# Kernel tuning notes

Hardware: AMD Instinct MI355X
Metric: run time of the kernel (lower is better)

The kernel has to match this reference:

```python
import jax, jax.numpy as jnp
import numpy as np

N_NODE = 20000
N_EDGE = 200000
EMBED = 256
PAIR = 128
HEADS = 16
HEAD_DIM = EMBED // HEADS
SCALING = HEAD_DIM ** -0.5
EPS = 1e-5


def _ln(x, w, b):
    m = x.mean(-1, keepdims=True)
    v = ((x - m) ** 2).mean(-1, keepdims=True)
    return (x - m) / jnp.sqrt(v + EPS) * w + b


def setup_inputs() -> dict:
    key = jax.random.key(0)
    ks = jax.random.split(key, 12)
    inp = {
        "query": jax.random.normal(ks[0], (N_NODE, EMBED), jnp.float32),
        "edge_index": jax.random.randint(ks[1], (N_EDGE, 2), 0, N_NODE, jnp.int64 if jax.config.jax_enable_x64 else jnp.int32),
        "edge_diff": jax.random.normal(ks[2], (N_EDGE, 3), jnp.float32),
        "pair": jax.random.normal(ks[3], (N_EDGE, PAIR), jnp.float32),
        "ln_w": jnp.ones((EMBED,), jnp.float32),
        "ln_b": jnp.zeros((EMBED,), jnp.float32),
        "pln_w": jnp.ones((PAIR,), jnp.float32),
        "pln_b": jnp.zeros((PAIR,), jnp.float32),
        "Wq": jax.random.normal(ks[4], (EMBED, EMBED), jnp.float32) * 0.02,
        "Wk": jax.random.normal(ks[5], (EMBED, EMBED), jnp.float32) * 0.02,
        "Wv": jax.random.normal(ks[6], (EMBED, EMBED), jnp.float32) * 0.02,
        "Wb": jax.random.normal(ks[7], (HEADS, PAIR), jnp.float32) * 0.02,
        "bb": jnp.zeros((HEADS,), jnp.float32),
        "Wf1": jax.random.normal(ks[8], (1, EMBED), jnp.float32) * 0.02,
        "bf1": jnp.zeros((1,), jnp.float32),
        "Wf2": jax.random.normal(ks[9], (1, EMBED), jnp.float32) * 0.02,
        "bf2": jnp.zeros((1,), jnp.float32),
        "Wf3": jax.random.normal(ks[10], (1, EMBED), jnp.float32) * 0.02,
        "bf3": jnp.zeros((1,), jnp.float32),
    }
    return inp


def reference(query, edge_index, edge_diff, pair, ln_w, ln_b, pln_w, pln_b,
              Wq, Wk, Wv, Wb, bb, Wf1, bf1, Wf2, bf2, Wf3, bf3):
    n_node = query.shape[0]
    src = edge_index[:, 0]
    dst = edge_index[:, 1]

    qn = _ln(query, ln_w, ln_b)          # preln on node features
    pn = _ln(pair, pln_w, pln_b)         # preln on pair features

    q = (qn @ Wq.T).reshape(n_node, HEADS, HEAD_DIM)
    k = (qn @ Wk.T).reshape(n_node, HEADS, HEAD_DIM)
    v = (qn @ Wv.T).reshape(n_node, HEADS, HEAD_DIM)

    qe = q[src] * SCALING                # [E,H,D]
    ke = k[dst]
    ve = v[dst]

    logits = (qe * ke).sum(-1) + pn @ Wb.T + bb   # [E,H]

    # segment softmax over destination node (edge_index[:,0])
    seg_max = jax.ops.segment_max(logits, src, num_segments=n_node)  # [N,H]
    ex = jnp.exp(logits - seg_max[src])
    denom = jax.ops.segment_sum(ex, src, num_segments=n_node)
    probs = ex / denom[src]              # [E,H]

    # 3D-weighted scatter-sum: out[n,h,c,d] = sum_e probs[e,h]*diff[e,c]*v[e,h,d]
    w = probs[:, :, None] * edge_diff[:, None, :]                    # [E,H,3]
    contrib = w[:, :, :, None] * ve[:, :, None, :]                   # [E,H,3,D]
    x = jax.ops.segment_sum(contrib, src, num_segments=n_node)       # [N,H,3,D]
    x = x.transpose(0, 2, 1, 3).reshape(n_node, 3, EMBED)            # [N,3,H*D]

    f1 = x[:, 0, :] @ Wf1.T + bf1
    f2 = x[:, 1, :] @ Wf2.T + bf2
    f3 = x[:, 2, :] @ Wf3.T + bf3
    return jnp.concatenate([f1, f2, f3], axis=-1).astype(jnp.float32)
```

## Files before the change

kernel.cpp:

```cpp
#include <hip/hip_runtime.h>
#include <math.h>

#define N_NODE 20000
#define N_EDGE 200000
#define EMBED 256
#define PAIR 128
#define HEADS 16
#define HEAD_DIM 16
#define SCALING 0.25f
#define LNEPS 1e-5f

typedef unsigned short u16;
typedef unsigned int u32;
typedef __attribute__((ext_vector_type(8))) short bf16x8;
typedef __attribute__((ext_vector_type(4))) float f32x4;

#define WS_QKV   0
#define WS_QN    30720000
#define WS_WBF   40960000
#define WS_WW    41353216
#define WS_C0    41357312
#define WS_C1    41357376
#define WS_BIAS  41357440
#define WS_VW    54157440
#define WS_CNT   57997440
#define WS_CUR   58077440
#define WS_OFF   58157440
#define WS_DE    58237504

__device__ __forceinline__ u16 f2bf(float f) {
  u32 u = __float_as_uint(f);
  u32 r = (u + 0x7FFFu + ((u >> 16) & 1u)) >> 16;
  return (u16)r;
}
__device__ __forceinline__ float bl(u32 u) { return __uint_as_float(u << 16); }
__device__ __forceinline__ float bh(u32 u) { return __uint_as_float(u & 0xFFFF0000u); }

__device__ __forceinline__ float dot8(uint4 a, uint4 b) {
  float s = bl(a.x) * bl(b.x) + bh(a.x) * bh(b.x);
  s += bl(a.y) * bl(b.y) + bh(a.y) * bh(b.y);
  s += bl(a.z) * bl(b.z) + bh(a.z) * bh(b.z);
  s += bl(a.w) * bl(b.w) + bh(a.w) * bh(b.w);
  return s;
}

__global__ __launch_bounds__(256) void k1_pre_kernel(
    const float* __restrict__ query, const float* __restrict__ ln_w,
    const float* __restrict__ ln_b, u16* __restrict__ qn,
    int* __restrict__ counts, int* __restrict__ cur,
    const float* __restrict__ Wq, const float* __restrict__ Wk,
    const float* __restrict__ Wv, u16* __restrict__ Wbf,
    const float* __restrict__ pln_w, const float* __restrict__ pln_b,
    const float* __restrict__ Wb, const float* __restrict__ bb,
    u16* __restrict__ WWbf, float* __restrict__ c0, float* __restrict__ c1) {
  int bid = blockIdx.x;
  if (bid < 5000) {
    int z = bid * 256 + threadIdx.x;
    if (z < N_NODE) { counts[z] = 0; cur[z] = 0; }
    int node = bid * 4 + (threadIdx.x >> 6);
    int lane = threadIdx.x & 63;
    float4 a = *(const float4*)(query + (size_t)node * EMBED + lane * 4);
    float s = a.x + a.y + a.z + a.w;
    float s2 = a.x * a.x + a.y * a.y + a.z * a.z + a.w * a.w;
    #pragma unroll
    for (int off = 32; off > 0; off >>= 1) {
      s += __shfl_xor(s, off);
      s2 += __shfl_xor(s2, off);
    }
    float m = s * (1.0f / EMBED);
    float r = rsqrtf(s2 * (1.0f / EMBED) - m * m + LNEPS);
    float4 w4 = *(const float4*)(ln_w + lane * 4);
    float4 b4 = *(const float4*)(ln_b + lane * 4);
    ushort4 st;
    st.x = f2bf((a.x - m) * r * w4.x + b4.x);
    st.y = f2bf((a.y - m) * r * w4.y + b4.y);
    st.z = f2bf((a.z - m) * r * w4.z + b4.z);
    st.w = f2bf((a.w - m) * r * w4.w + b4.w);
    *(ushort4*)(qn + (size_t)node * EMBED + lane * 4) = st;
  } else if (bid < 5192) {
    int g4 = (bid - 5000) * 256 + threadIdx.x;
    int idx = g4 * 4;
    const float* src = (idx < 65536) ? Wq : (idx < 131072 ? Wk : Wv);
    float4 v = *(const float4*)(src + (idx & 65535));
    ushort4 st = {f2bf(v.x), f2bf(v.y), f2bf(v.z), f2bf(v.w)};
    *(ushort4*)(Wbf + idx) = st;
  } else if (threadIdx.x < 64) {
    int l = threadIdx.x;
    for (int h = 0; h < HEADS; h++) {
      int i0 = l * 2;
      float wb0 = Wb[h * PAIR + i0], wb1 = Wb[h * PAIR + i0 + 1];
      float ww0 = pln_w[i0] * wb0, ww1 = pln_w[i0 + 1] * wb1;
      WWbf[h * PAIR + i0] = f2bf(ww0);
      WWbf[h * PAIR + i0 + 1] = f2bf(ww1);
      float s1 = ww0 + ww1;
      float s0 = pln_b[i0] * wb0 + pln_b[i0 + 1] * wb1;
      #pragma unroll
      for (int off = 32; off > 0; off >>= 1) {
        s1 += __shfl_xor(s1, off);
        s0 += __shfl_xor(s0, off);
      }
      if (l == 0) {
        c1[h] = s1;
        c0[h] = s0 + bb[h];
      }
    }
  }
}

#define GP 264
__global__ __launch_bounds__(256, 2) void k2_gemm_hist_kernel(
    const u16* __restrict__ qn, const u16* __restrict__ Wbf,
    u16* __restrict__ qkv, const int* __restrict__ edge_index,
    int* __restrict__ counts) {
  __shared__ u16 As[64 * GP];
  __shared__ u16 Bs[64 * GP];
  int bid = blockIdx.x;
  if (bid >= 3756) {
    int e = (bid - 3756) * 256 + threadIdx.x;
    if (e < N_EDGE) atomicAdd(&counts[edge_index[e * 2]], 1);
    return;
  }
  int bx = bid % 313, by = bid / 313;
  int t = threadIdx.x;
  int wv = t >> 6, lane = t & 63;
  int quad = lane >> 4, l16 = lane & 15;
  int row0 = bx * 64, col0 = by * 64;
  #pragma unroll
  for (int j = 0; j < 8; j++) {
    int row = j * 8 + (t >> 5);
    int slot = t & 31;
    int ra = min(row0 + row, N_NODE - 1);
    uint4 va = *(const uint4*)(qn + (size_t)ra * 256 + slot * 8);
    *(uint4*)(&As[row * GP + slot * 8]) = va;
    uint4 vb = *(const uint4*)(Wbf + (size_t)(col0 + row) * 256 + slot * 8);
    *(uint4*)(&Bs[row * GP + slot * 8]) = vb;
  }
  __syncthreads();
  int mt = (wv >> 1) * 32, nt = (wv & 1) * 32;
  f32x4 acc[2][2];
  #pragma unroll
  for (int im = 0; im < 2; im++)
    #pragma unroll
    for (int in_ = 0; in_ < 2; in_++) acc[im][in_] = (f32x4){0.f, 0.f, 0.f, 0.f};
  #pragma unroll
  for (int sk = 0; sk < 8; sk++) {
    int ko = sk * 32 + quad * 8;
    bf16x8 a0 = *(const bf16x8*)(&As[(mt + l16) * GP + ko]);
    bf16x8 a1 = *(const bf16x8*)(&As[(mt + 16 + l16) * GP + ko]);
    bf16x8 b0 = *(const bf16x8*)(&Bs[(nt + l16) * GP + ko]);
    bf16x8 b1 = *(const bf16x8*)(&Bs[(nt + 16 + l16) * GP + ko]);
    acc[0][0] = __builtin_amdgcn_mfma_f32_16x16x32_bf16(a0, b0, acc[0][0], 0, 0, 0);
    acc[0][1] = __builtin_amdgcn_mfma_f32_16x16x32_bf16(a0, b1, acc[0][1], 0, 0, 0);
    acc[1][0] = __builtin_amdgcn_mfma_f32_16x16x32_bf16(a1, b0, acc[1][0], 0, 0, 0);
    acc[1][1] = __builtin_amdgcn_mfma_f32_16x16x32_bf16(a1, b1, acc[1][1], 0, 0, 0);
  }
  float scale = (col0 < 256) ? SCALING : 1.0f;
  #pragma unroll
  for (int im = 0; im < 2; im++) {
    #pragma unroll
    for (int in_ = 0; in_ < 2; in_++) {
      #pragma unroll
      for (int r = 0; r < 4; r++) {
        int grow = row0 + mt + im * 16 + quad * 4 + r;
        int gcol = col0 + nt + in_ * 16 + l16;
        if (grow < N_NODE)
          qkv[(size_t)grow * 768 + gcol] = f2bf(acc[im][in_][r] * scale);
      }
    }
  }
}

__global__ __launch_bounds__(1024) void scan_kernel(
    const int* __restrict__ counts, int* __restrict__ off) {
  __shared__ int part[1024];
  int t = threadIdx.x;
  int loc[20];
  int s = 0;
  #pragma unroll
  for (int i = 0; i < 20; i++) {
    int idx = t * 20 + i;
    int v = (idx < N_NODE) ? counts[idx] : 0;
    loc[i] = s;
    s += v;
  }
  part[t] = s;
  __syncthreads();
  int x = s;
  for (int o = 1; o < 1024; o <<= 1) {
    int y = (t >= o) ? part[t - o] : 0;
    __syncthreads();
    x += y;
    part[t] = x;
    __syncthreads();
  }
  int excl = x - s;
  #pragma unroll
  for (int i = 0; i < 20; i++) {
    int idx = t * 20 + i;
    if (idx < N_NODE) off[idx] = excl + loc[i];
  }
  if (t == 0) off[N_NODE] = N_EDGE;
}

#define PP 136
__global__ __launch_bounds__(256) void k4_bias_vw_scatter_kernel(
    const float* __restrict__ pair, const u16* __restrict__ WWbf,
    const float* __restrict__ c0g, const float* __restrict__ c1g,
    float* __restrict__ bias, const u16* __restrict__ qkv,
    const float* __restrict__ Wf1, const float* __restrict__ Wf2,
    const float* __restrict__ Wf3, float* __restrict__ vw,
    const int* __restrict__ edge_index, const int* __restrict__ off,
    int* __restrict__ cur, int2* __restrict__ de) {
  __shared__ u16 Ps[64 * PP];
  __shared__ u16 WWs[16 * PP];
  __shared__ float ms[64], rs[64], c0s[16], c1s[16];
  int bid = blockIdx.x;
  int t = threadIdx.x;
  if (bid >= 4375) {
    int e = (bid - 4375) * 256 + t;
    if (e < N_EDGE) {
      int src = edge_index[e * 2 + 0];
      int dst = edge_index[e * 2 + 1];
      int pos = off[src] + atomicAdd(&cur[src], 1);
      de[pos] = make_int2(dst, e);
    }
    return;
  }
  if (bid >= 3125) {
    int gid = (bid - 3125) * 256 + t;
    int n = gid >> 4, h = gid & 15;
    const uint4* vp = (const uint4*)(qkv + (size_t)n * 768 + 512 + h * 16);
    uint4 va = vp[0], vb = vp[1];
    float v[16];
    v[0] = bl(va.x); v[1] = bh(va.x); v[2] = bl(va.y); v[3] = bh(va.y);
    v[4] = bl(va.z); v[5] = bh(va.z); v[6] = bl(va.w); v[7] = bh(va.w);
    v[8] = bl(vb.x); v[9] = bh(vb.x); v[10] = bl(vb.y); v[11] = bh(vb.y);
    v[12] = bl(vb.z); v[13] = bh(vb.z); v[14] = bl(vb.w); v[15] = bh(vb.w);
    const float* wf[3] = {Wf1 + h * 16, Wf2 + h * 16, Wf3 + h * 16};
    #pragma unroll
    for (int c = 0; c < 3; c++) {
      float s = 0.f;
      #pragma unroll
      for (int d = 0; d < 16; d++) s += v[d] * wf[c][d];
      vw[(size_t)n * 48 + h * 3 + c] = s;
    }
    return;
  }
  int wv = t >> 6, lane = t & 63;
  int quad = lane >> 4, l16 = lane & 15;
  int e0 = bid * 64;
  #pragma unroll
  for (int j = 0; j < 8; j++) {
    int L = j * 256 + t;
    int row = L >> 5, slot = L & 31;
    float4 p = *(const float4*)(pair + (size_t)(e0 + row) * PAIR + slot * 4);
    ushort4 st = {f2bf(p.x), f2bf(p.y), f2bf(p.z), f2bf(p.w)};
    *(ushort4*)(&Ps[row * PP + slot * 4]) = st;
  }
  #pragma unroll
  for (int j = 0; j < 2; j++) {
    int L = j * 256 + t;
    int row = L >> 5, slot = L & 31;
    ushort4 w = *(const ushort4*)(WWbf + row * PAIR + slot * 4);
    *(ushort4*)(&WWs[row * PP + slot * 4]) = w;
  }
  if (t < 16) {
    c0s[t] = c0g[t];
    c1s[t] = c1g[t];
  }
  __syncthreads();
  {
    int row = t >> 2, qq = t & 3;
    float s = 0.f, s2 = 0.f;
    #pragma unroll
    for (int jj = 0; jj < 8; jj++) {
      ushort4 u = *(const ushort4*)(&Ps[row * PP + (qq * 8 + jj) * 4]);
      float x0 = __uint_as_float((u32)u.x << 16);
      float x1 = __uint_as_float((u32)u.y << 16);
      float x2 = __uint_as_float((u32)u.z << 16);
      float x3 = __uint_as_float((u32)u.w << 16);
      s += x0 + x1 + x2 + x3;
      s2 += x0 * x0 + x1 * x1 + x2 * x2 + x3 * x3;
    }
    s += __shfl_xor(s, 1); s += __shfl_xor(s, 2);
    s2 += __shfl_xor(s2, 1); s2 += __shfl_xor(s2, 2);
    if (qq == 0) {
      float m = s * (1.0f / PAIR);
      ms[row] = m;
      rs[row] = rsqrtf(s2 * (1.0f / PAIR) - m * m + LNEPS);
    }
  }
  __syncthreads();
  f32x4 acc = (f32x4){0.f, 0.f, 0.f, 0.f};
  #pragma unroll
  for (int sk = 0; sk < 4; sk++) {
    int ko = sk * 32 + quad * 8;
    bf16x8 a = *(const bf16x8*)(&Ps[(wv * 16 + l16) * PP + ko]);
    bf16x8 b = *(const bf16x8*)(&WWs[l16 * PP + ko]);
    acc = __builtin_amdgcn_mfma_f32_16x16x32_bf16(a, b, acc, 0, 0, 0);
  }
  #pragma unroll
  for (int r = 0; r < 4; r++) {
    int el = wv * 16 + quad * 4 + r;
    float bv = rs[el] * (acc[r] - ms[el] * c1s[l16]) + c0s[l16];
    bias[(size_t)(e0 + el) * HEADS + l16] = bv;
  }
}

__global__ __launch_bounds__(256) void seg_attn_kernel(
    const u16* __restrict__ qkv, const float* __restrict__ bias,
    const int* __restrict__ off, const int2* __restrict__ de,
    const float* __restrict__ vw, const float* __restrict__ edge_diff,
    const float* __restrict__ bf1, const float* __restrict__ bf2,
    const float* __restrict__ bf3, float* __restrict__ out) {
  int wv = threadIdx.x >> 6, lane = threadIdx.x & 63;
  int src = blockIdx.x * 4 + wv;
  int h = lane & 15, eslot = lane >> 4;
  int lo = off[src];
  int deg = off[src + 1] - lo;
  const uint4* qp = (const uint4*)(qkv + (size_t)src * 768 + h * 16);
  uint4 q0 = qp[0], q1 = qp[1];
  float exsum = 0.f, a0 = 0.f, a1 = 0.f, a2 = 0.f;
  for (int ei = eslot; ei < deg; ei += 4) {
    int2 d_e = de[lo + ei];
    const uint4* kp = (const uint4*)(qkv + (size_t)d_e.x * 768 + 256 + h * 16);
    float d = dot8(q0, kp[0]) + dot8(q1, kp[1]);
    float ex = __expf(d + bias[(size_t)d_e.y * HEADS + h]);
    exsum += ex;
    const float* vp = vw + (size_t)d_e.x * 48 + h * 3;
    const float* dp = edge_diff + (size_t)d_e.y * 3;
    a0 += ex * vp[0] * dp[0];
    a1 += ex * vp[1] * dp[1];
    a2 += ex * vp[2] * dp[2];
  }
  exsum += __shfl_xor(exsum, 16);
  exsum += __shfl_xor(exsum, 32);
  float rden = (exsum > 0.f) ? 1.0f / exsum : 0.f;
  a0 *= rden; a1 *= rden; a2 *= rden;
  #pragma unroll
  for (int o = 1; o < 64; o <<= 1) {
    a0 += __shfl_xor(a0, o);
    a1 += __shfl_xor(a1, o);
    a2 += __shfl_xor(a2, o);
  }
  if (lane == 0) {
    out[src * 3 + 0] = a0 + bf1[0];
    out[src * 3 + 1] = a1 + bf2[0];
    out[src * 3 + 2] = a2 + bf3[0];
  }
}

extern "C" void kernel_launch(void* const* d_in, const int* in_sizes, int n_in,
                              void* d_out, int out_size, void* d_ws,
                              size_t ws_size, hipStream_t stream) {
  const float* query      = (const float*)d_in[0];
  const int*   edge_index = (const int*)d_in[1];
  const float* edge_diff  = (const float*)d_in[2];
  const float* pair       = (const float*)d_in[3];
  const float* ln_w       = (const float*)d_in[4];
  const float* ln_b       = (const float*)d_in[5];
  const float* pln_w      = (const float*)d_in[6];
  const float* pln_b      = (const float*)d_in[7];
  const float* Wq         = (const float*)d_in[8];
  const float* Wk         = (const float*)d_in[9];
  const float* Wv         = (const float*)d_in[10];
  const float* Wb         = (const float*)d_in[11];
  const float* bb         = (const float*)d_in[12];
  const float* Wf1        = (const float*)d_in[13];
  const float* bf1        = (const float*)d_in[14];
  const float* Wf2        = (const float*)d_in[15];
  const float* bf2        = (const float*)d_in[16];
  const float* Wf3        = (const float*)d_in[17];
  const float* bf3        = (const float*)d_in[18];

  char* ws = (char*)d_ws;
  u16*   qkv   = (u16*)(ws + WS_QKV);
  u16*   qn    = (u16*)(ws + WS_QN);
  u16*   Wbf   = (u16*)(ws + WS_WBF);
  u16*   WWbf  = (u16*)(ws + WS_WW);
  float* c0    = (float*)(ws + WS_C0);
  float* c1    = (float*)(ws + WS_C1);
  float* bias  = (float*)(ws + WS_BIAS);
  float* vw    = (float*)(ws + WS_VW);
  int*   counts= (int*)(ws + WS_CNT);
  int*   cur   = (int*)(ws + WS_CUR);
  int*   off   = (int*)(ws + WS_OFF);
  int2*  de    = (int2*)(ws + WS_DE);
  float* out   = (float*)d_out;

  k1_pre_kernel<<<5193, 256, 0, stream>>>(query, ln_w, ln_b, qn, counts, cur,
                                          Wq, Wk, Wv, Wbf, pln_w, pln_b, Wb,
                                          bb, WWbf, c0, c1);
  k2_gemm_hist_kernel<<<4538, 256, 0, stream>>>(qn, Wbf, qkv, edge_index,
                                                counts);
  scan_kernel<<<1, 1024, 0, stream>>>(counts, off);
  k4_bias_vw_scatter_kernel<<<5157, 256, 0, stream>>>(
      pair, WWbf, c0, c1, bias, qkv, Wf1, Wf2, Wf3, vw, edge_index, off, cur,
      de);
  seg_attn_kernel<<<N_NODE / 4, 256, 0, stream>>>(qkv, bias, off, de, vw,
                                                  edge_diff, bf1, bf2, bf3,
                                                  out);
}
```

Baseline: 295.8 us.

## Retile QKV GEMM to 128x128 blocks with K-loop staging

Replaces the 64x64-tile GEMM, which staged the full K=256 at once, with 128x128 output tiles. K is processed in four 64-wide chunks staged through smaller shared buffers, and each wave computes a 4x4 grid of MFMA tiles. This raises operand reuse per shared-memory load and cuts the GEMM block count from 3756 to 942, which lowers redundant global reads of qn and the weights. The trade-offs are more accumulator registers, extra syncs per K step, and fewer blocks to fill the GPU.

```diff
diff --git a/kernel.cpp b/kernel.cpp
--- a/kernel.cpp
+++ b/kernel.cpp
@@ -107,62 +107,73 @@
   }
 }
 
-#define GP 264
+#define BKP 72
 __global__ __launch_bounds__(256, 2) void k2_gemm_hist_kernel(
     const u16* __restrict__ qn, const u16* __restrict__ Wbf,
     u16* __restrict__ qkv, const int* __restrict__ edge_index,
     int* __restrict__ counts) {
-  __shared__ u16 As[64 * GP];
-  __shared__ u16 Bs[64 * GP];
+  __shared__ u16 As[128 * BKP];
+  __shared__ u16 Bs[128 * BKP];
   int bid = blockIdx.x;
-  if (bid >= 3756) {
-    int e = (bid - 3756) * 256 + threadIdx.x;
+  if (bid >= 942) {
+    int e = (bid - 942) * 256 + threadIdx.x;
     if (e < N_EDGE) atomicAdd(&counts[edge_index[e * 2]], 1);
     return;
   }
-  int bx = bid % 313, by = bid / 313;
+  int bx = bid % 157, by = bid / 157;
   int t = threadIdx.x;
   int wv = t >> 6, lane = t & 63;
   int quad = lane >> 4, l16 = lane & 15;
-  int row0 = bx * 64, col0 = by * 64;
-  #pragma unroll
-  for (int j = 0; j < 8; j++) {
-    int row = j * 8 + (t >> 5);
-    int slot = t & 31;
-    int ra = min(row0 + row, N_NODE - 1);
-    uint4 va = *(const uint4*)(qn + (size_t)ra * 256 + slot * 8);
-    *(uint4*)(&As[row * GP + slot * 8]) = va;
-    uint4 vb = *(const uint4*)(Wbf + (size_t)(col0 + row) * 256 + slot * 8);
-    *(uint4*)(&Bs[row * GP + slot * 8]) = vb;
-  }
-  __syncthreads();
-  int mt = (wv >> 1) * 32, nt = (wv & 1) * 32;
-  f32x4 acc[2][2];
-  #pragma unroll
-  for (int im = 0; im < 2; im++)
-    #pragma unroll
-    for (int in_ = 0; in_ < 2; in_++) acc[im][in_] = (f32x4){0.f, 0.f, 0.f, 0.f};
-  #pragma unroll
-  for (int sk = 0; sk < 8; sk++) {
-    int ko = sk * 32 + quad * 8;
-    bf16x8 a0 = *(const bf16x8*)(&As[(mt + l16) * GP + ko]);
-    bf16x8 a1 = *(const bf16x8*)(&As[(mt + 16 + l16) * GP + ko]);
-    bf16x8 b0 = *(const bf16x8*)(&Bs[(nt + l16) * GP + ko]);
-    bf16x8 b1 = *(const bf16x8*)(&Bs[(nt + 16 + l16) * GP + ko]);
-    acc[0][0] = __builtin_amdgcn_mfma_f32_16x16x32_bf16(a0, b0, acc[0][0], 0, 0, 0);
-    acc[0][1] = __builtin_amdgcn_mfma_f32_16x16x32_bf16(a0, b1, acc[0][1], 0, 0, 0);
-    acc[1][0] = __builtin_amdgcn_mfma_f32_16x16x32_bf16(a1, b0, acc[1][0], 0, 0, 0);
-    acc[1][1] = __builtin_amdgcn_mfma_f32_16x16x32_bf16(a1, b1, acc[1][1], 0, 0, 0);
-  }
-  float scale = (col0 < 256) ? SCALING : 1.0f;
-  #pragma unroll
-  for (int im = 0; im < 2; im++) {
-    #pragma unroll
-    for (int in_ = 0; in_ < 2; in_++) {
+  int row0 = bx * 128, col0 = by * 128;
+  int mt = (wv >> 1) * 64, nt = (wv & 1) * 64;
+
+  f32x4 acc[4][4];
+  #pragma unroll
+  for (int im = 0; im < 4; im++)
+    #pragma unroll
+    for (int in_ = 0; in_ < 4; in_++) acc[im][in_] = (f32x4){0.f, 0.f, 0.f, 0.f};
+
+  for (int it = 0; it < 4; it++) {
+    int k0 = it * 64;
+    #pragma unroll
+    for (int j = 0; j < 4; j++) {
+      int L = j * 256 + t;
+      int row = L >> 3, slot = L & 7;
+      int ra = min(row0 + row, N_NODE - 1);
+      uint4 va = *(const uint4*)(qn + (size_t)ra * 256 + k0 + slot * 8);
+      *(uint4*)(&As[row * BKP + slot * 8]) = va;
+      uint4 vb = *(const uint4*)(Wbf + (size_t)(col0 + row) * 256 + k0 + slot * 8);
+      *(uint4*)(&Bs[row * BKP + slot * 8]) = vb;
+    }
+    __syncthreads();
+    #pragma unroll
+    for (int s = 0; s < 2; s++) {
+      int ko = s * 32 + quad * 8;
+      bf16x8 af[4], bf[4];
+      #pragma unroll
+      for (int im = 0; im < 4; im++)
+        af[im] = *(const bf16x8*)(&As[(mt + im * 16 + l16) * BKP + ko]);
+      #pragma unroll
+      for (int in_ = 0; in_ < 4; in_++)
+        bf[in_] = *(const bf16x8*)(&Bs[(nt + in_ * 16 + l16) * BKP + ko]);
+      #pragma unroll
+      for (int im = 0; im < 4; im++)
+        #pragma unroll
+        for (int in_ = 0; in_ < 4; in_++)
+          acc[im][in_] = __builtin_amdgcn_mfma_f32_16x16x32_bf16(
+              af[im], bf[in_], acc[im][in_], 0, 0, 0);
+    }
+    __syncthreads();
+  }
+  #pragma unroll
+  for (int im = 0; im < 4; im++) {
+    #pragma unroll
+    for (int in_ = 0; in_ < 4; in_++) {
+      int gcol = col0 + nt + in_ * 16 + l16;
+      float scale = (gcol < 256) ? SCALING : 1.0f;
       #pragma unroll
       for (int r = 0; r < 4; r++) {
         int grow = row0 + mt + im * 16 + quad * 4 + r;
-        int gcol = col0 + nt + in_ * 16 + l16;
         if (grow < N_NODE)
           qkv[(size_t)grow * 768 + gcol] = f2bf(acc[im][in_][r] * scale);
       }
@@ -391,7 +402,7 @@
   k1_pre_kernel<<<5193, 256, 0, stream>>>(query, ln_w, ln_b, qn, counts, cur,
                                           Wq, Wk, Wv, Wbf, pln_w, pln_b, Wb,
                                           bb, WWbf, c0, c1);
-  k2_gemm_hist_kernel<<<4538, 256, 0, stream>>>(qn, Wbf, qkv, edge_index,
+  k2_gemm_hist_kernel<<<1724, 256, 0, stream>>>(qn, Wbf, qkv, edge_index,
                                                 counts);
   scan_kernel<<<1, 1024, 0, stream>>>(counts, off);
   k4_bias_vw_scatter_kernel<<<5157, 256, 0, stream>>>(
```

After: 290.1 us. Within noise of the previous version (-1.9%).
